# Performance work log

Measured on AMD Instinct MI355X. Metric: run time of the kernel, lower is better.

The kernel has to match this reference:

```python
import jax, jax.numpy as jnp
import numpy as np

D = 1024
H = 16
HD = D // H
EPS = 1e-8


def setup_inputs() -> dict:
    key = jax.random.key(0)
    ks = jax.random.split(key, 12)
    B, S = 2, 2048
    scale = 1.0 / np.sqrt(D)
    inp = {
        "x": jax.random.normal(ks[0], (B, S, D), dtype=jnp.float32),
        "M": jax.random.uniform(ks[1], (B, S, S), dtype=jnp.float32),
        "Wq": jax.random.normal(ks[2], (D, D), dtype=jnp.float32) * scale,
        "bq": jax.random.normal(ks[3], (D,), dtype=jnp.float32) * 0.01,
        "Wk": jax.random.normal(ks[4], (D, D), dtype=jnp.float32) * scale,
        "bk": jax.random.normal(ks[5], (D,), dtype=jnp.float32) * 0.01,
        "Wv": jax.random.normal(ks[6], (D, D), dtype=jnp.float32) * scale,
        "bv": jax.random.normal(ks[7], (D,), dtype=jnp.float32) * 0.01,
        "Wo": jax.random.normal(ks[8], (D, D), dtype=jnp.float32) * scale,
        "bo": jax.random.normal(ks[9], (D,), dtype=jnp.float32) * 0.01,
    }
    return inp


def reference(x, M, Wq, bq, Wk, bk, Wv, bv, Wo, bo):
    B, S, _ = x.shape
    sm_scale = HD ** -0.5
    # projections (torch Linear: x @ W^T + b), split into heads: [B,H,S,HD]
    def proj(W, b):
        return (x @ W.T + b).reshape(B, S, H, HD).transpose(0, 2, 1, 3)
    Q, K, V = proj(Wq, bq), proj(Wk, bk), proj(Wv, bv)
    # scores: [B,H,S,S], gated pre-softmax by M broadcast over heads
    scores = jnp.einsum("bhqd,bhkd->bhqk", Q, K) * sm_scale
    Mb = M[:, None, :, :]  # [B,1,S,S]
    scores = scores * Mb
    attn = jax.nn.softmax(scores, axis=-1)
    # post-softmax re-gate + L1 renormalize
    A_sparse = attn * Mb
    norm = jnp.sum(jnp.abs(A_sparse), axis=-1, keepdims=True) + EPS
    A_bar = A_sparse / norm
    out = jnp.einsum("bhqk,bhkd->bhqd", A_bar, V)
    out = out.transpose(0, 2, 1, 3).reshape(B, S, D)
    return out @ Wo.T + bo
```

## Files before the change

### kernel.cpp

```cpp
#include <hip/hip_runtime.h>
#include <hip/hip_bf16.h>
#include <stdint.h>

#define S_LEN 2048
#define D_DIM 1024
#define NROW 4096

typedef __attribute__((ext_vector_type(8))) short short8;
typedef __attribute__((ext_vector_type(4))) float f32x4;
typedef __attribute__((ext_vector_type(4))) int i32x4;
typedef unsigned short ushort_t;

__device__ __forceinline__ ushort_t f2bf(float f) {
  uint32_t u = __float_as_uint(f);
  u += 0x7fffu + ((u >> 16) & 1u);
  return (ushort_t)(u >> 16);
}

__device__ __forceinline__ void gload16(const void* g, void* l) {
  __builtin_amdgcn_global_load_lds((const __attribute__((address_space(1))) void*)g,
                                   (__attribute__((address_space(3))) void*)l, 16, 0, 0);
}

__global__ void convert4_kernel(const float* __restrict__ x,
                                const float* __restrict__ wq, const float* __restrict__ wk,
                                const float* __restrict__ wv,
                                ushort_t* __restrict__ xb, ushort_t* __restrict__ wcat) {
  const float* src; ushort_t* dst; int n;
  switch (blockIdx.y) {
    case 0: src = x;  dst = xb;             n = NROW * D_DIM;  break;
    case 1: src = wq; dst = wcat;           n = D_DIM * D_DIM; break;
    case 2: src = wk; dst = wcat + 1048576; n = D_DIM * D_DIM; break;
    default: src = wv; dst = wcat + 2097152; n = D_DIM * D_DIM; break;
  }
  int base = (blockIdx.x * 256 + threadIdx.x) * 8;
  if (base >= n) return;
  f32x4 va = *(const f32x4*)(src + base);
  f32x4 vb = *(const f32x4*)(src + base + 4);
  short8 o;
  o[0] = (short)f2bf(va[0]); o[1] = (short)f2bf(va[1]);
  o[2] = (short)f2bf(va[2]); o[3] = (short)f2bf(va[3]);
  o[4] = (short)f2bf(vb[0]); o[5] = (short)f2bf(vb[1]);
  o[6] = (short)f2bf(vb[2]); o[7] = (short)f2bf(vb[3]);
  *(short8*)(dst + base) = o;
}

__global__ void convert_wo_kernel(const float* __restrict__ wo, ushort_t* __restrict__ wob) {
  int base = (blockIdx.x * 256 + threadIdx.x) * 8;
  f32x4 va = *(const f32x4*)(wo + base);
  f32x4 vb = *(const f32x4*)(wo + base + 4);
  short8 o;
  o[0] = (short)f2bf(va[0]); o[1] = (short)f2bf(va[1]);
  o[2] = (short)f2bf(va[2]); o[3] = (short)f2bf(va[3]);
  o[4] = (short)f2bf(vb[0]); o[5] = (short)f2bf(vb[1]);
  o[6] = (short)f2bf(vb[2]); o[7] = (short)f2bf(vb[3]);
  *(short8*)(wob + base) = o;
}

template<int MODE>
__global__ __launch_bounds__(256, 4) void gemm_glds(const ushort_t* __restrict__ A,
                                                    const ushort_t* __restrict__ Bw,
                                                    const float* __restrict__ bias0,
                                                    const float* __restrict__ bias1,
                                                    const float* __restrict__ bias2,
                                                    void* __restrict__ Cout) {
  __shared__ ushort_t As[128 * 64];
  __shared__ ushort_t Bs[128 * 64];
  const int t = threadIdx.x;
  const int lane = t & 63;
  const int w = t >> 6;
  const int wm = w >> 1, wn = w & 1;
  const int m0 = blockIdx.x * 128, n0 = blockIdx.y * 128;
  const int g = lane >> 4, c0 = lane & 15;
  const int srow = lane >> 3, scol = (lane & 7) * 8;

  f32x4 acc[4][4] = {};

  for (int kt = 0; kt < 16; ++kt) {
    const int kk = kt * 64;
#pragma unroll
    for (int i = 0; i < 4; ++i) {
      gload16(A  + (size_t)(m0 + w * 32 + i * 8 + srow) * D_DIM + kk + scol, &As[(w * 32 + i * 8) * 64]);
      gload16(Bw + (size_t)(n0 + w * 32 + i * 8 + srow) * D_DIM + kk + scol, &Bs[(w * 32 + i * 8) * 64]);
    }
    asm volatile("s_waitcnt vmcnt(0)" ::: "memory");
    __syncthreads();
#pragma unroll
    for (int kc = 0; kc < 2; ++kc) {
      short8 af[4], bf[4];
#pragma unroll
      for (int mf = 0; mf < 4; ++mf)
        af[mf] = *(const short8*)&As[(wm * 64 + mf * 16 + c0) * 64 + kc * 32 + g * 8];
#pragma unroll
      for (int nf = 0; nf < 4; ++nf)
        bf[nf] = *(const short8*)&Bs[(wn * 64 + nf * 16 + c0) * 64 + kc * 32 + g * 8];
#pragma unroll
      for (int mf = 0; mf < 4; ++mf)
#pragma unroll
        for (int nf = 0; nf < 4; ++nf)
          acc[mf][nf] = __builtin_amdgcn_mfma_f32_16x16x32_bf16(af[mf], bf[nf], acc[mf][nf], 0, 0, 0);
    }
    __syncthreads();
  }

#pragma unroll
  for (int nf = 0; nf < 4; ++nf) {
    int jj = n0 + wn * 64 + nf * 16 + c0;
    float bval;
    if (MODE == 0) {
      int proj = jj >> 10, jcol = jj & 1023;
      const float* bp = (proj == 0) ? bias0 : ((proj == 1) ? bias1 : bias2);
      bval = bp[jcol];
    } else {
      bval = bias0[jj];
    }
#pragma unroll
    for (int mf = 0; mf < 4; ++mf) {
#pragma unroll
      for (int r = 0; r < 4; ++r) {
        int ii = m0 + wm * 64 + mf * 16 + g * 4 + r;
        float v = acc[mf][nf][r] + bval;
        if (MODE == 2) {
          ((float*)Cout)[(size_t)ii * D_DIM + jj] = v;
        } else {
          int proj = jj >> 10, jcol = jj & 1023;
          if (proj == 0) v *= 0.125f;
          int bb = ii >> 11, s = ii & 2047;
          size_t addr;
          if (proj < 2) {
            int hcol = jcol >> 6, hd = jcol & 63;
            addr = (size_t)proj * 4194304 + ((size_t)(bb * 16 + hcol) * 2048 + s) * 64 + hd;
          } else {
            addr = (size_t)2 * 4194304 + ((size_t)bb * 1024 + jcol) * 2048 + s;
          }
          ((ushort_t*)Cout)[addr] = f2bf(v);
        }
      }
    }
  }
}

__global__ __launch_bounds__(256, 4) void attn_kernel(const ushort_t* __restrict__ Qg,
                                                      const ushort_t* __restrict__ Kg,
                                                      const ushort_t* __restrict__ Vtg,
                                                      const float* __restrict__ Mg,
                                                      ushort_t* __restrict__ aout) {
  __shared__ ushort_t Ks[64 * 72];
  __shared__ ushort_t Vts[64 * 72];

  const int t = threadIdx.x, lane = t & 63, w = t >> 6;
  const int g = lane >> 4, c0 = lane & 15;
  const int id = blockIdx.x;
  const int xcd = id & 7, j = id >> 3;
  const int hh = j & 15, gi = j >> 4;
  const int g64 = xcd + 8 * gi;
  const int b = g64 >> 5, q0 = (g64 & 31) * 64;
  const int bh = b * 16 + hh;

  const ushort_t* Qbase  = Qg  + ((size_t)bh * 2048 + q0) * 64;
  const ushort_t* Kbase  = Kg  + (size_t)bh * 2048 * 64;
  const ushort_t* Vtbase = Vtg + (size_t)bh * 64 * 2048;
  const float*    Mbase  = Mg + ((size_t)b * 2048 + q0 + w * 16 + c0) * 2048 + g * 4;

  short8 qf[2];
#pragma unroll
  for (int kc = 0; kc < 2; ++kc)
    qf[kc] = *(const short8*)(Qbase + (size_t)(w * 16 + c0) * 64 + kc * 32 + g * 8);

  f32x4 o[4] = {};
  float dpe = 0.f;
  const int idxA = (((g & 1) * 2 + (g >> 1)) * 16 + c0) * 4;
  const int idxB = (((g & 1) * 2 + 1 - (g >> 1)) * 16 + c0) * 4;
  const bool glo = (g < 2);
  const bool gb = (g & 1);

  short8 rk[2], rv[2];
#define A_LOAD(kt) { const int k0 = (kt) * 64; \
    _Pragma("unroll") for (int i = 0; i < 2; ++i) { int c = i * 256 + t; int row = c >> 3, c8 = (c & 7) * 8; \
      rk[i] = *(const short8*)(Kbase  + (size_t)(k0 + row) * 64 + c8); \
      rv[i] = *(const short8*)(Vtbase + (size_t)row * 2048 + k0 + c8); } }
#define A_WRITE() { \
    _Pragma("unroll") for (int i = 0; i < 2; ++i) { int c = i * 256 + t; int row = c >> 3, c8 = (c & 7) * 8; \
      *(short8*)&Ks[row * 72 + c8]  = rk[i]; \
      *(short8*)&Vts[row * 72 + c8] = rv[i]; } }

  A_LOAD(0); A_WRITE(); __syncthreads();

  for (int kt = 0; kt < 32; ++kt) {
    if (kt < 31) A_LOAD(kt + 1);

    f32x4 mv[4];
    {
      const float* Mk = Mbase + kt * 64;
#pragma unroll
      for (int nf = 0; nf < 4; ++nf)
        mv[nf] = *(const f32x4*)(Mk + nf * 16);
    }

    f32x4 sf[4] = {};
#pragma unroll
    for (int kc = 0; kc < 2; ++kc) {
      short8 kf[4];
#pragma unroll
      for (int nf = 0; nf < 4; ++nf)
        kf[nf] = *(const short8*)&Ks[(nf * 16 + c0) * 72 + kc * 32 + g * 8];
#pragma unroll
      for (int nf = 0; nf < 4; ++nf)
        sf[nf] = __builtin_amdgcn_mfma_f32_16x16x32_bf16(kf[nf], qf[kc], sf[nf], 0, 0, 0);
    }

    uint32_t w4[4][2];
#pragma unroll
    for (int nf = 0; nf < 4; ++nf) {
      float p[4];
#pragma unroll
      for (int r = 0; r < 4; ++r) {
        float m = mv[nf][r];
        float e = __expf(sf[nf][r] * m);
        float pe = m * e;
        dpe += pe;
        p[r] = pe;
      }
      asm("v_cvt_pk_bf16_f32 %0, %1, %2" : "=v"(w4[nf][0]) : "v"(p[0]), "v"(p[1]));
      asm("v_cvt_pk_bf16_f32 %0, %1, %2" : "=v"(w4[nf][1]) : "v"(p[2]), "v"(p[3]));
    }

    short8 pf[2];
#pragma unroll
    for (int kc = 0; kc < 2; ++kc) {
      uint32_t sA0 = gb ? w4[2 * kc + 1][0] : w4[2 * kc][0];
      uint32_t sA1 = gb ? w4[2 * kc + 1][1] : w4[2 * kc][1];
      uint32_t sB0 = gb ? w4[2 * kc][0]     : w4[2 * kc + 1][0];
      uint32_t sB1 = gb ? w4[2 * kc][1]     : w4[2 * kc + 1][1];
      uint32_t rA0 = (uint32_t)__builtin_amdgcn_ds_bpermute(idxA, (int)sA0);
      uint32_t rA1 = (uint32_t)__builtin_amdgcn_ds_bpermute(idxA, (int)sA1);
      uint32_t rB0 = (uint32_t)__builtin_amdgcn_ds_bpermute(idxB, (int)sB0);
      uint32_t rB1 = (uint32_t)__builtin_amdgcn_ds_bpermute(idxB, (int)sB1);
      i32x4 f4;
      f4[0] = (int)(glo ? rA0 : rB0);
      f4[1] = (int)(glo ? rA1 : rB1);
      f4[2] = (int)(glo ? rB0 : rA0);
      f4[3] = (int)(glo ? rB1 : rA1);
      pf[kc] = __builtin_bit_cast(short8, f4);
    }

#pragma unroll
    for (int kc = 0; kc < 2; ++kc) {
#pragma unroll
      for (int df = 0; df < 4; ++df) {
        short8 vf = *(const short8*)&Vts[(df * 16 + c0) * 72 + kc * 32 + g * 8];
        o[df] = __builtin_amdgcn_mfma_f32_16x16x32_bf16(vf, pf[kc], o[df], 0, 0, 0);
      }
    }

    __syncthreads();
    if (kt < 31) {
      A_WRITE();
      __syncthreads();
    }
  }

  dpe += __shfl_xor(dpe, 16);
  dpe += __shfl_xor(dpe, 32);
  float inv = 1.0f / dpe;

#pragma unroll
  for (int df = 0; df < 4; ++df) {
    float v0 = o[df][0] * inv, v1 = o[df][1] * inv;
    float v2 = o[df][2] * inv, v3 = o[df][3] * inv;
    uint32_t d0, d1;
    asm("v_cvt_pk_bf16_f32 %0, %1, %2" : "=v"(d0) : "v"(v0), "v"(v1));
    asm("v_cvt_pk_bf16_f32 %0, %1, %2" : "=v"(d1) : "v"(v2), "v"(v3));
    unsigned long long pk = (unsigned long long)d0 | ((unsigned long long)d1 << 32);
    *(unsigned long long*)&aout[((size_t)b * 2048 + q0 + w * 16 + c0) * 1024 + hh * 64 + df * 16 + g * 4] = pk;
  }
#undef A_LOAD
#undef A_WRITE
}

extern "C" void kernel_launch(void* const* d_in, const int* in_sizes, int n_in,
                              void* d_out, int out_size, void* d_ws, size_t ws_size,
                              hipStream_t stream) {
  const float* x  = (const float*)d_in[0];
  const float* M  = (const float*)d_in[1];
  const float* Wq = (const float*)d_in[2];
  const float* bq = (const float*)d_in[3];
  const float* Wk = (const float*)d_in[4];
  const float* bk = (const float*)d_in[5];
  const float* Wv = (const float*)d_in[6];
  const float* bv = (const float*)d_in[7];
  const float* Wo = (const float*)d_in[8];
  const float* bo = (const float*)d_in[9];
  float* out = (float*)d_out;
  char* ws = (char*)d_ws;

  ushort_t* Qb    = (ushort_t*)(ws);
  ushort_t* Kb    = (ushort_t*)(ws + 8388608);
  ushort_t* Vtb   = (ushort_t*)(ws + 16777216);
  ushort_t* xb    = (ushort_t*)(ws + 25165824);
  ushort_t* Wcat  = (ushort_t*)(ws + 33554432);
  ushort_t* aoutb = (ushort_t*)(ws + 41943040);
  ushort_t* wob   = (ushort_t*)(ws + 39845888);

  convert4_kernel<<<dim3(2048, 4), 256, 0, stream>>>(x, Wq, Wk, Wv, xb, Wcat);
  convert_wo_kernel<<<512, 256, 0, stream>>>(Wo, wob);
  gemm_glds<0><<<dim3(32, 24), 256, 0, stream>>>(xb, Wcat, bq, bk, bv, (void*)Qb);
  attn_kernel<<<1024, 256, 0, stream>>>(Qb, Kb, Vtb, M, aoutb);
  gemm_glds<2><<<dim3(32, 8), 256, 0, stream>>>(aoutb, wob, bo, bo, bo, (void*)out);
}
```

Measured before the change: 158.4 us.

## Double-buffer attention K/V via direct global-to-LDS loads with XOR swizzle

```diff
diff --git a/kernel.cpp b/kernel.cpp
--- a/kernel.cpp
+++ b/kernel.cpp
@@ -127,11 +127,16 @@
           if (proj == 0) v *= 0.125f;
           int bb = ii >> 11, s = ii & 2047;
           size_t addr;
-          if (proj < 2) {
+          if (proj == 0) {
             int hcol = jcol >> 6, hd = jcol & 63;
-            addr = (size_t)proj * 4194304 + ((size_t)(bb * 16 + hcol) * 2048 + s) * 64 + hd;
+            addr = ((size_t)(bb * 16 + hcol) * 2048 + s) * 64 + hd;
+          } else if (proj == 1) {
+            int hcol = jcol >> 6, hd = jcol & 63;
+            addr = (size_t)4194304 + ((size_t)(bb * 16 + hcol) * 2048 + s) * 64
+                 + (hd ^ ((s & 7) << 3));
           } else {
-            addr = (size_t)2 * 4194304 + ((size_t)bb * 1024 + jcol) * 2048 + s;
+            addr = (size_t)8388608 + ((size_t)bb * 1024 + jcol) * 2048
+                 + (s ^ ((jcol & 7) << 3));
           }
           ((ushort_t*)Cout)[addr] = f2bf(v);
         }
@@ -140,27 +145,28 @@
   }
 }
 
-__global__ __launch_bounds__(256, 4) void attn_kernel(const ushort_t* __restrict__ Qg,
+__global__ __launch_bounds__(512, 4) void attn_kernel(const ushort_t* __restrict__ Qg,
                                                       const ushort_t* __restrict__ Kg,
                                                       const ushort_t* __restrict__ Vtg,
                                                       const float* __restrict__ Mg,
                                                       ushort_t* __restrict__ aout) {
-  __shared__ ushort_t Ks[64 * 72];
-  __shared__ ushort_t Vts[64 * 72];
+  __shared__ ushort_t Ks[2][64 * 64];
+  __shared__ ushort_t Vts[2][64 * 64];
 
   const int t = threadIdx.x, lane = t & 63, w = t >> 6;
   const int g = lane >> 4, c0 = lane & 15;
   const int id = blockIdx.x;
-  const int xcd = id & 7, j = id >> 3;
-  const int hh = j & 15, gi = j >> 4;
-  const int g64 = xcd + 8 * gi;
-  const int b = g64 >> 5, q0 = (g64 & 31) * 64;
+  const int r8 = id & 7, hh = (id >> 3) & 15, ss = id >> 7;
+  const int combo = r8 + 8 * ss, b = combo >> 4, q0 = (combo & 15) * 128;
   const int bh = b * 16 + hh;
 
-  const ushort_t* Qbase  = Qg  + ((size_t)bh * 2048 + q0) * 64;
-  const ushort_t* Kbase  = Kg  + (size_t)bh * 2048 * 64;
-  const ushort_t* Vtbase = Vtg + (size_t)bh * 64 * 2048;
-  const float*    Mbase  = Mg + ((size_t)b * 2048 + q0 + w * 16 + c0) * 2048 + g * 4;
+  const ushort_t* Qbase = Qg + ((size_t)bh * 2048 + q0) * 64;
+  const float*    Mbase = Mg + ((size_t)b * 2048 + q0 + w * 16 + c0) * 2048 + g * 4;
+
+  const ushort_t* Ksrc = Kg  + (size_t)bh * 2048 * 64
+                       + ((size_t)(w * 8 + (lane >> 3)) * 64 + (lane & 7) * 8);
+  const ushort_t* Vsrc = Vtg + (size_t)bh * 64 * 2048
+                       + ((size_t)(w * 8 + (lane >> 3)) * 2048 + (lane & 7) * 8);
 
   short8 qf[2];
 #pragma unroll
@@ -168,46 +174,49 @@
     qf[kc] = *(const short8*)(Qbase + (size_t)(w * 16 + c0) * 64 + kc * 32 + g * 8);
 
   f32x4 o[4] = {};
-  float dpe = 0.f;
+  f32x4 dpev = {0.f, 0.f, 0.f, 0.f};
+  const int swz = (c0 & 7) << 3;
   const int idxA = (((g & 1) * 2 + (g >> 1)) * 16 + c0) * 4;
   const int idxB = (((g & 1) * 2 + 1 - (g >> 1)) * 16 + c0) * 4;
   const bool glo = (g < 2);
   const bool gb = (g & 1);
 
-  short8 rk[2], rv[2];
-#define A_LOAD(kt) { const int k0 = (kt) * 64; \
-    _Pragma("unroll") for (int i = 0; i < 2; ++i) { int c = i * 256 + t; int row = c >> 3, c8 = (c & 7) * 8; \
-      rk[i] = *(const short8*)(Kbase  + (size_t)(k0 + row) * 64 + c8); \
-      rv[i] = *(const short8*)(Vtbase + (size_t)row * 2048 + k0 + c8); } }
-#define A_WRITE() { \
-    _Pragma("unroll") for (int i = 0; i < 2; ++i) { int c = i * 256 + t; int row = c >> 3, c8 = (c & 7) * 8; \
-      *(short8*)&Ks[row * 72 + c8]  = rk[i]; \
-      *(short8*)&Vts[row * 72 + c8] = rv[i]; } }
-
-  A_LOAD(0); A_WRITE(); __syncthreads();
+#define STAGE(kt_, buf_) { \
+    gload16(Ksrc + (size_t)(kt_) * 4096, &Ks[buf_][w * 512]); \
+    gload16(Vsrc + (size_t)(kt_) * 64,   &Vts[buf_][w * 512]); }
+
+  STAGE(0, 0);
+  f32x4 rm[4];
+#pragma unroll
+  for (int nf = 0; nf < 4; ++nf) rm[nf] = *(const f32x4*)(Mbase + nf * 16);
+  asm volatile("s_waitcnt vmcnt(0)" ::: "memory");
+  __builtin_amdgcn_s_barrier();
+  __builtin_amdgcn_sched_barrier(0);
 
   for (int kt = 0; kt < 32; ++kt) {
-    if (kt < 31) A_LOAD(kt + 1);
-
-    f32x4 mv[4];
-    {
-      const float* Mk = Mbase + kt * 64;
-#pragma unroll
-      for (int nf = 0; nf < 4; ++nf)
-        mv[nf] = *(const f32x4*)(Mk + nf * 16);
+    const int cur = kt & 1;
+    f32x4 rmn[4];
+    if (kt < 31) {
+      STAGE(kt + 1, cur ^ 1);
+      __builtin_amdgcn_sched_barrier(0);
+      const float* Mk = Mbase + (size_t)(kt + 1) * 64;
+#pragma unroll
+      for (int nf = 0; nf < 4; ++nf) rmn[nf] = *(const f32x4*)(Mk + nf * 16);
     }
 
     f32x4 sf[4] = {};
+    __builtin_amdgcn_s_setprio(1);
 #pragma unroll
     for (int kc = 0; kc < 2; ++kc) {
       short8 kf[4];
 #pragma unroll
       for (int nf = 0; nf < 4; ++nf)
-        kf[nf] = *(const short8*)&Ks[(nf * 16 + c0) * 72 + kc * 32 + g * 8];
+        kf[nf] = *(const short8*)&Ks[cur][(nf * 16 + c0) * 64 + ((kc * 32 + g * 8) ^ swz)];
 #pragma unroll
       for (int nf = 0; nf < 4; ++nf)
         sf[nf] = __builtin_amdgcn_mfma_f32_16x16x32_bf16(kf[nf], qf[kc], sf[nf], 0, 0, 0);
     }
+    __builtin_amdgcn_s_setprio(0);
 
     uint32_t w4[4][2];
 #pragma unroll
@@ -215,10 +224,10 @@
       float p[4];
 #pragma unroll
       for (int r = 0; r < 4; ++r) {
-        float m = mv[nf][r];
+        float m = rm[nf][r];
         float e = __expf(sf[nf][r] * m);
         float pe = m * e;
-        dpe += pe;
+        dpev[r] += pe;
         p[r] = pe;
       }
       asm("v_cvt_pk_bf16_f32 %0, %1, %2" : "=v"(w4[nf][0]) : "v"(p[0]), "v"(p[1]));
@@ -244,22 +253,27 @@
       pf[kc] = __builtin_bit_cast(short8, f4);
     }
 
+    __builtin_amdgcn_s_setprio(1);
 #pragma unroll
     for (int kc = 0; kc < 2; ++kc) {
 #pragma unroll
       for (int df = 0; df < 4; ++df) {
-        short8 vf = *(const short8*)&Vts[(df * 16 + c0) * 72 + kc * 32 + g * 8];
+        short8 vf = *(const short8*)&Vts[cur][(df * 16 + c0) * 64 + ((kc * 32 + g * 8) ^ swz)];
         o[df] = __builtin_amdgcn_mfma_f32_16x16x32_bf16(vf, pf[kc], o[df], 0, 0, 0);
       }
     }
-
-    __syncthreads();
+    __builtin_amdgcn_s_setprio(0);
+
     if (kt < 31) {
-      A_WRITE();
-      __syncthreads();
-    }
-  }
-
+      asm volatile("s_waitcnt vmcnt(4)" ::: "memory");
+      __builtin_amdgcn_s_barrier();
+      __builtin_amdgcn_sched_barrier(0);
+#pragma unroll
+      for (int nf = 0; nf < 4; ++nf) rm[nf] = rmn[nf];
+    }
+  }
+
+  float dpe = (dpev[0] + dpev[1]) + (dpev[2] + dpev[3]);
   dpe += __shfl_xor(dpe, 16);
   dpe += __shfl_xor(dpe, 32);
   float inv = 1.0f / dpe;
@@ -274,8 +288,7 @@
     unsigned long long pk = (unsigned long long)d0 | ((unsigned long long)d1 << 32);
     *(unsigned long long*)&aout[((size_t)b * 2048 + q0 + w * 16 + c0) * 1024 + hh * 64 + df * 16 + g * 4] = pk;
   }
-#undef A_LOAD
-#undef A_WRITE
+#undef STAGE
 }
 
 extern "C" void kernel_launch(void* const* d_in, const int* in_sizes, int n_in,
@@ -305,6 +318,6 @@
   convert4_kernel<<<dim3(2048, 4), 256, 0, stream>>>(x, Wq, Wk, Wv, xb, Wcat);
   convert_wo_kernel<<<512, 256, 0, stream>>>(Wo, wob);
   gemm_glds<0><<<dim3(32, 24), 256, 0, stream>>>(xb, Wcat, bq, bk, bv, (void*)Qb);
-  attn_kernel<<<1024, 256, 0, stream>>>(Qb, Kb, Vtb, M, aoutb);
+  attn_kernel<<<512, 512, 0, stream>>>(Qb, Kb, Vtb, M, aoutb);
   gemm_glds<2><<<dim3(32, 8), 256, 0, stream>>>(aoutb, wob, bo, bo, bo, (void*)out);
 }
```

Result: faster. 151.1 us (-4.6%).
